# Kernel optimization log

Measured on AMD Instinct MI355X. Metric: run time of the kernel, lower is better.

Reference implementation:

```python
import jax, jax.numpy as jnp
import numpy as np

N_ATOMS = 8192
N_PAIRS = 65536
F = 128        # n_atombasis
R = 20         # n_radialbasis
B = 5          # graph_n_blocks
EPS = 1e-8     # stability constant


def setup_inputs() -> dict:
    key = jax.random.key(0)
    ks = jax.random.split(key, 16)
    rn = lambda k, shape, s=0.05: jax.random.normal(k, shape, dtype=jnp.float32) * s
    return {
        "features": jax.random.normal(ks[0], (N_ATOMS, F), jnp.float32),
        "distances": jax.random.uniform(ks[1], (N_PAIRS,), jnp.float32, 0.5, 5.0),
        "vectors": jax.random.normal(ks[2], (N_PAIRS, 3), jnp.float32),
        "cutoffs": jax.random.uniform(ks[3], (N_PAIRS,), jnp.float32),
        "rbfs": jax.random.normal(ks[4], (N_PAIRS, R), jnp.float32),
        "filter_W": rn(ks[5], (R, B * 3 * F)),
        "filter_b": jnp.zeros((B * 3 * F,), jnp.float32),
        "int_W1": rn(ks[6], (B, F, F)),
        "int_b1": jnp.zeros((B, F), jnp.float32),
        "int_W2": rn(ks[7], (B, F, 3 * F)),
        "int_b2": jnp.zeros((B, 3 * F), jnp.float32),
        "mix_Wv": rn(ks[8], (B, F, 2 * F)),
        "mix_W1": rn(ks[9], (B, 2 * F, F)),
        "mix_b1": jnp.zeros((B, F), jnp.float32),
        "mix_W2": rn(ks[10], (B, F, 3 * F)),
        "mix_b2": jnp.zeros((B, 3 * F), jnp.float32),
        "idx_i": jax.random.randint(ks[11], (N_PAIRS,), 0, N_ATOMS),
        "idx_j": jax.random.randint(ks[12], (N_PAIRS,), 0, N_ATOMS),
    }


def reference(features, distances, vectors, cutoffs, rbfs,
              filter_W, filter_b, int_W1, int_b1, int_W2, int_b2,
              mix_Wv, mix_W1, mix_b1, mix_W2, mix_b2, idx_i, idx_j):
    n_atoms = features.shape[0]
    # Cutoff-weighted radial filters, one (3F) chunk per block: [P, B*3F]
    descriptors = (rbfs @ filter_W + filter_b) * cutoffs[:, None]
    dir_ij = vectors / distances[:, None]                       # [P, 3]

    q = features[:, None, :]                                    # [N, 1, F]
    mu = jnp.zeros((n_atoms, 3, F), dtype=features.dtype)       # [N, 3, F]

    for b in range(B):
        # --- interaction block ---
        x = jax.nn.silu(q @ int_W1[b] + int_b1[b]) @ int_W2[b] + int_b2[b]  # [N,1,3F]
        Wij = descriptors[:, None, b * 3 * F:(b + 1) * 3 * F]               # [P,1,3F]
        xj = x[idx_j] * Wij                                                 # [P,1,3F]
        muj = mu[idx_j]                                                     # [P,3,F]
        dq, dmuR, dmumu = jnp.split(xj, 3, axis=-1)                         # [P,1,F] each
        dmu = dmuR * dir_ij[:, :, None] + dmumu * muj                       # [P,3,F]
        q = q + jax.ops.segment_sum(dq, idx_i, num_segments=n_atoms)
        mu = mu + jax.ops.segment_sum(dmu, idx_i, num_segments=n_atoms)

        # --- mixing block ---
        mu_V, mu_W = jnp.split(mu @ mix_Wv[b], 2, axis=-1)                  # [N,3,F] each
        mu_Vn = jnp.sqrt(jnp.sum(mu_V ** 2, axis=-2, keepdims=True) + EPS)  # [N,1,F]
        ctx = jnp.concatenate([q, mu_Vn], axis=-1)                          # [N,1,2F]
        y = jax.nn.silu(ctx @ mix_W1[b] + mix_b1[b]) @ mix_W2[b] + mix_b2[b]
        dq_i, dmu_i, dqmu_i = jnp.split(y, 3, axis=-1)                      # [N,1,F] each
        q = q + dq_i + dqmu_i * jnp.sum(mu_V * mu_W, axis=1, keepdims=True)
        mu = mu + dmu_i * mu_W

    return q[:, 0, :], mu
```

## Files before the change

### kernel.cpp

```cpp
#include <hip/hip_runtime.h>
#include <hip/hip_bf16.h>

#define NA 8192
#define NP 65536
#define WROW 1920

typedef short short8 __attribute__((ext_vector_type(8)));
typedef short short4v __attribute__((ext_vector_type(4)));
typedef float floatx4 __attribute__((ext_vector_type(4)));
typedef unsigned uint3v __attribute__((ext_vector_type(3)));

static __device__ __forceinline__ short f2bf(float f) {
    union { float f; unsigned u; } v; v.f = f;
    unsigned r = v.u + 0x7FFF + ((v.u >> 16) & 1);
    return (short)(r >> 16);
}
static __device__ __forceinline__ float bf2f(short s) {
    union { unsigned u; float f; } v;
    v.u = ((unsigned)(unsigned short)s) << 16;
    return v.f;
}
static __device__ __forceinline__ unsigned char f2fp8(float f) {
    int p = __builtin_amdgcn_cvt_pk_fp8_f32(f, 0.f, 0, false);
    return (unsigned char)(p & 0xFF);
}
static __device__ __forceinline__ float fp82f(unsigned char b) {
    return __builtin_amdgcn_cvt_f32_fp8((int)b, 0);
}
static __device__ __forceinline__ float silu(float v) {
    return v / (1.f + __expf(-v));
}

static __device__ __forceinline__ void swz(const float* __restrict__ src,
                                           short* __restrict__ dst,
                                           int K, int N, int idx) {
    int kn = K * N;
    int b = idx / kn;
    int r = idx - b * kn;
    int tile = r >> 9, li = r & 511;
    int lane = li >> 3, bb = li & 7;
    int Kt = K >> 5;
    int nt = tile / Kt, kt = tile - nt * Kt;
    int k = kt * 32 + (lane >> 4) * 8 + bb;
    int n = nt * 16 + (lane & 15);
    dst[idx] = f2bf(src[b * kn + k * N + n]);
}

__global__ __launch_bounds__(256) void k_tconv_all(const float* __restrict__ iW1,
                                                   const float* __restrict__ iW2,
                                                   const float* __restrict__ mWv,
                                                   const float* __restrict__ mW1,
                                                   const float* __restrict__ mW2,
                                                   const float* __restrict__ fW,
                                                   short* __restrict__ W1t,
                                                   short* __restrict__ W2t,
                                                   short* __restrict__ Wvt,
                                                   short* __restrict__ mW1t,
                                                   short* __restrict__ mW2t,
                                                   short* __restrict__ fWt) {
    int idx = blockIdx.x * 256 + threadIdx.x;
    if (idx < 81920)       { swz(iW1, W1t, 128, 128, idx); return; }
    idx -= 81920;
    if (idx < 245760)      { swz(iW2, W2t, 128, 384, idx); return; }
    idx -= 245760;
    if (idx < 163840)      { swz(mWv, Wvt, 128, 256, idx); return; }
    idx -= 163840;
    if (idx < 163840)      { swz(mW1, mW1t, 256, 128, idx); return; }
    idx -= 163840;
    if (idx < 245760)      { swz(mW2, mW2t, 128, 384, idx); return; }
    idx -= 245760;
    if (idx < 61440) {
        int b = idx / 12288;
        int r = idx - b * 12288;
        int nt = r >> 9;
        int li = r & 511;
        int lane = li >> 3, bb = li & 7;
        int k = (lane >> 4) * 8 + bb;
        int n = nt * 16 + (lane & 15);
        fWt[idx] = (k < 20) ? f2bf(fW[k * WROW + b * 384 + n]) : (short)0;
    }
}

__global__ __launch_bounds__(256) void k_init(const float* __restrict__ feat,
                                              float* __restrict__ q,
                                              float* __restrict__ mu,
                                              short* __restrict__ q_bf,
                                              unsigned* __restrict__ xmu_u,
                                              int* __restrict__ counts,
                                              int* __restrict__ cursor,
                                              float* __restrict__ cut_csr,
                                              short* __restrict__ rbf_c) {
    int idx = blockIdx.x * 256 + threadIdx.x;
    if (idx < NA * 128) { float v = feat[idx]; q[idx] = v; q_bf[idx] = f2bf(v); }
    mu[idx] = 0.f;
    xmu_u[idx] = 0;
    if (idx < NA) { counts[idx] = 0; cursor[idx] = 0; }
    if (idx < 16) {
        cut_csr[NP + idx] = 0.f;
        #pragma unroll
        for (int k = 0; k < 32; ++k) rbf_c[(NP + idx) * 32 + k] = 0;
    }
}

__global__ __launch_bounds__(256) void k_hist(const int* __restrict__ idx_i,
                                              int* __restrict__ counts) {
    int p = blockIdx.x * 256 + threadIdx.x;
    if (p < NP) atomicAdd(&counts[idx_i[p]], 1);
}

__global__ __launch_bounds__(1024) void k_scan(const int* __restrict__ counts,
                                               int* __restrict__ offs) {
    __shared__ int sums[1024];
    int t = threadIdx.x;
    int local[8];
    int s = 0;
    #pragma unroll
    for (int k = 0; k < 8; ++k) { local[k] = s; s += counts[t * 8 + k]; }
    sums[t] = s;
    __syncthreads();
    for (int off = 1; off < 1024; off <<= 1) {
        int v = sums[t];
        int u = (t >= off) ? sums[t - off] : 0;
        __syncthreads();
        sums[t] = v + u;
        __syncthreads();
    }
    int base = (t > 0) ? sums[t - 1] : 0;
    #pragma unroll
    for (int k = 0; k < 8; ++k) offs[t * 8 + k] = base + local[k];
    if (t == 1023) offs[NA] = sums[1023];
}

__global__ __launch_bounds__(256) void k_fillprep(const int* __restrict__ idx_i,
                                                  const int* __restrict__ idx_j,
                                                  const int* __restrict__ offs,
                                                  int* __restrict__ cursor,
                                                  const float* __restrict__ cut,
                                                  const float* __restrict__ dist,
                                                  const float* __restrict__ vec,
                                                  const float* __restrict__ rbfs,
                                                  int* __restrict__ jcsr,
                                                  float* __restrict__ cut_csr,
                                                  float4* __restrict__ dir_csr,
                                                  short* __restrict__ rbf_c) {
    int p = blockIdx.x * 256 + threadIdx.x;
    if (p >= NP) return;
    int i = idx_i[p];
    int pos = atomicAdd(&cursor[i], 1);
    int e = offs[i] + pos;
    jcsr[e] = idx_j[p];
    float c = cut[p];
    cut_csr[e] = c;
    float invd = 1.f / dist[p];
    float4 d;
    d.x = vec[p * 3 + 0] * invd;
    d.y = vec[p * 3 + 1] * invd;
    d.z = vec[p * 3 + 2] * invd;
    d.w = 0.f;
    dir_csr[e] = d;
    #pragma unroll
    for (int k = 0; k < 20; ++k) rbf_c[e * 32 + k] = f2bf(rbfs[p * 20 + k] * c);
    #pragma unroll
    for (int k = 20; k < 32; ++k) rbf_c[e * 32 + k] = 0;
}

__global__ __launch_bounds__(256) void k_x(const short* __restrict__ q_bf,
                                           const short* __restrict__ W1sw,
                                           const short* __restrict__ W2sw,
                                           const float* __restrict__ b1,
                                           const float* __restrict__ b2,
                                           unsigned char* __restrict__ xmu) {
    __shared__ __align__(16) short qtile[16 * 136];
    __shared__ __align__(16) short hs[16 * 136];
    int t = threadIdx.x;
    int wv = t >> 6, lane = t & 63, quad = lane >> 4, l16 = lane & 15;
    int a0 = blockIdx.x * 16;

    #pragma unroll
    for (int it = 0; it < 2; ++it) {
        int c = it * 256 + t;
        int row = c >> 5, col4 = c & 31;
        *(short4v*)(qtile + row * 136 + col4 * 4) =
            *(const short4v*)(q_bf + (a0 + row) * 128 + col4 * 4);
    }
    __syncthreads();

    floatx4 acc0 = {0.f, 0.f, 0.f, 0.f}, acc1 = {0.f, 0.f, 0.f, 0.f};
    #pragma unroll
    for (int kk = 0; kk < 4; ++kk) {
        short8 a  = *(const short8*)(qtile + l16 * 136 + kk * 32 + quad * 8);
        short8 b0 = *(const short8*)(W1sw + ((wv * 2 + 0) * 4 + kk) * 512 + lane * 8);
        short8 bq = *(const short8*)(W1sw + ((wv * 2 + 1) * 4 + kk) * 512 + lane * 8);
        acc0 = __builtin_amdgcn_mfma_f32_16x16x32_bf16(a, b0, acc0, 0, 0, 0);
        acc1 = __builtin_amdgcn_mfma_f32_16x16x32_bf16(a, bq, acc1, 0, 0, 0);
    }
    __syncthreads();
    {
        int n0 = wv * 32 + l16;
        float bia0 = b1[n0], bia1 = b1[n0 + 16];
        #pragma unroll
        for (int r = 0; r < 4; ++r) {
            int m = quad * 4 + r;
            hs[m * 136 + n0]      = f2bf(silu(acc0[r] + bia0));
            hs[m * 136 + n0 + 16] = f2bf(silu(acc1[r] + bia1));
        }
    }
    __syncthreads();
    floatx4 acc[6];
    #pragma unroll
    for (int jj = 0; jj < 6; ++jj) acc[jj] = {0.f, 0.f, 0.f, 0.f};
    #pragma unroll
    for (int kk = 0; kk < 4; ++kk) {
        short8 a = *(const short8*)(hs + l16 * 136 + kk * 32 + quad * 8);
        #pragma unroll
        for (int jj = 0; jj < 6; ++jj) {
            short8 b = *(const short8*)(W2sw + ((wv * 6 + jj) * 4 + kk) * 512 + lane * 8);
            acc[jj] = __builtin_amdgcn_mfma_f32_16x16x32_bf16(a, b, acc[jj], 0, 0, 0);
        }
    }
    #pragma unroll
    for (int jj = 0; jj < 6; ++jj) {
        int n = wv * 96 + jj * 16 + l16;
        float bia = b2[n];
        #pragma unroll
        for (int r = 0; r < 4; ++r) {
            int m = quad * 4 + r;
            xmu[(size_t)((a0 + m) * 128 + (n & 127)) * 12 + (n >> 7)] =
                f2fp8(acc[jj][r] + bia);
        }
    }
}

__global__ __launch_bounds__(256, 6) void k_gather(const unsigned char* __restrict__ xmu,
                                                   const short* __restrict__ rbf_c,
                                                   const short* __restrict__ fWt,
                                                   const float* __restrict__ fbp,
                                                   const int* __restrict__ jcsr,
                                                   const float* __restrict__ cut_csr,
                                                   const float4* __restrict__ dir_csr,
                                                   const int* __restrict__ offs,
                                                   short* __restrict__ dqg,
                                                   short* __restrict__ dmug) {
    __shared__ short dlds[16 * 392];
    __shared__ float pm[4 * 128];
    int i = blockIdx.x;
    int t = threadIdx.x;
    int h = t >> 7;
    int f = t & 127;
    int wv = t >> 6, lane = t & 63, quad = lane >> 4, l16 = lane & 15;
    int start = offs[i], end = offs[i + 1];
    float qa = 0.f, m0a = 0.f, m1a = 0.f, m2a = 0.f;

    for (int e0 = start; e0 < end; e0 += 16) {
        if (e0 > start) __syncthreads();
        short8 a = *(const short8*)(rbf_c + (e0 + l16) * 32 + quad * 8);
        float c0 = cut_csr[e0 + quad * 4 + 0];
        float c1 = cut_csr[e0 + quad * 4 + 1];
        float c2 = cut_csr[e0 + quad * 4 + 2];
        float c3 = cut_csr[e0 + quad * 4 + 3];
        #pragma unroll
        for (int nt = 0; nt < 6; ++nt) {
            int col = wv * 96 + nt * 16 + l16;
            short8 bfr = *(const short8*)(fWt + (wv * 6 + nt) * 512 + lane * 8);
            floatx4 z = {0.f, 0.f, 0.f, 0.f};
            floatx4 acc = __builtin_amdgcn_mfma_f32_16x16x32_bf16(a, bfr, z, 0, 0, 0);
            float fbv = fbp[col];
            dlds[(quad * 4 + 0) * 392 + col] = f2bf(acc[0] + fbv * c0);
            dlds[(quad * 4 + 1) * 392 + col] = f2bf(acc[1] + fbv * c1);
            dlds[(quad * 4 + 2) * 392 + col] = f2bf(acc[2] + fbv * c2);
            dlds[(quad * 4 + 3) * 392 + col] = f2bf(acc[3] + fbv * c3);
        }
        __syncthreads();
        int lim = (end < e0 + 16) ? end : (e0 + 16);
        int e = e0 + h;
        if (e < lim) {
            int jA = jcsr[e];
            float4 dirA = dir_csr[e];
            uint3v recA = *(const uint3v*)(xmu + (size_t)jA * 1536 + f * 12);
            for (; e < lim; e += 2) {
                uint3v rec = recA;
                float4 cdir = dirA;
                int en = e + 2;
                if (en < lim) {
                    int jn = jcsr[en];
                    dirA = dir_csr[en];
                    recA = *(const uint3v*)(xmu + (size_t)jn * 1536 + f * 12);
                }
                float x0 = fp82f((unsigned char)(rec.x & 0xFF));
                float x1 = fp82f((unsigned char)((rec.x >> 8) & 0xFF));
                float x2 = fp82f((unsigned char)((rec.x >> 16) & 0xFF));
                float u0 = bf2f((short)(rec.y & 0xFFFF));
                float u1 = bf2f((short)(rec.y >> 16));
                float u2 = bf2f((short)(rec.z & 0xFFFF));
                int le = e - e0;
                float wa = bf2f(dlds[le * 392 + f]);
                float wb = bf2f(dlds[le * 392 + 128 + f]);
                float wc = bf2f(dlds[le * 392 + 256 + f]);
                qa += x0 * wa;
                float xb = x1 * wb;
                float xc = x2 * wc;
                m0a += xb * cdir.x + xc * u0;
                m1a += xb * cdir.y + xc * u1;
                m2a += xb * cdir.z + xc * u2;
            }
        }
    }
    if (h == 1) {
        pm[0 * 128 + f] = qa;
        pm[1 * 128 + f] = m0a;
        pm[2 * 128 + f] = m1a;
        pm[3 * 128 + f] = m2a;
    }
    __syncthreads();
    if (h == 0) {
        qa  += pm[0 * 128 + f];
        m0a += pm[1 * 128 + f];
        m1a += pm[2 * 128 + f];
        m2a += pm[3 * 128 + f];
        dqg[i * 128 + f]             = f2bf(qa);
        dmug[(i * 3 + 0) * 128 + f]  = f2bf(m0a);
        dmug[(i * 3 + 1) * 128 + f]  = f2bf(m1a);
        dmug[(i * 3 + 2) * 128 + f]  = f2bf(m2a);
    }
}

__global__ __launch_bounds__(512, 6) void k_mixx(const float* __restrict__ mu_ro,
                                                 const short* __restrict__ dmug,
                                                 const float* __restrict__ q_ro,
                                                 const short* __restrict__ dqg,
                                                 const short* __restrict__ Wvsw,
                                                 const short* __restrict__ W1sw,
                                                 const short* __restrict__ W2sw,
                                                 const float* __restrict__ b1,
                                                 const float* __restrict__ b2,
                                                 float* __restrict__ q,
                                                 float* __restrict__ mu,
                                                 unsigned char* __restrict__ xmu,
                                                 const short* __restrict__ xW1sw,
                                                 const short* __restrict__ xW2sw,
                                                 const float* __restrict__ xb1,
                                                 const float* __restrict__ xb2,
                                                 int do_x) {
    __shared__ __align__(16) char smem[51968];
    short* ms    = (short*)(smem);
    short* qtile = (short*)(smem + 13056);
    short* Vv    = (short*)(smem + 17408);
    short* hs    = (short*)(smem + 17408);
    short* Vw    = (short*)(smem + 30464);
    short* vnb   = (short*)(smem + 43520);
    short* sb    = (short*)(smem + 47872);
    int t = threadIdx.x;
    int wv = t >> 6, lane = t & 63, quad = lane >> 4, l16 = lane & 15;
    int a0 = blockIdx.x * 16;

    #pragma unroll
    for (int k = 0; k < 12; ++k) {
        int idx = k * 512 + t;
        int row = idx >> 7, c = idx & 127;
        int g = (a0 * 3 + row) * 128 + c;
        ms[row * 136 + c] = f2bf(mu_ro[g] + bf2f(dmug[g]));
    }
    #pragma unroll
    for (int k = 0; k < 4; ++k) {
        int idx = k * 512 + t;
        int row = idx >> 7, c = idx & 127;
        int g = (a0 + row) * 128 + c;
        qtile[row * 136 + c] = f2bf(q_ro[g] + bf2f(dqg[g]));
    }
    __syncthreads();

    {
        floatx4 acc[3][2];
        #pragma unroll
        for (int mt = 0; mt < 3; ++mt)
            #pragma unroll
            for (int nt = 0; nt < 2; ++nt) acc[mt][nt] = {0.f, 0.f, 0.f, 0.f};
        #pragma unroll
        for (int kk = 0; kk < 4; ++kk) {
            short8 a[3];
            #pragma unroll
            for (int mt = 0; mt < 3; ++mt)
                a[mt] = *(const short8*)(ms + (mt * 16 + l16) * 136 + kk * 32 + quad * 8);
            #pragma unroll
            for (int nt = 0; nt < 2; ++nt) {
                short8 b = *(const short8*)(Wvsw + ((wv * 2 + nt) * 4 + kk) * 512 + lane * 8);
                #pragma unroll
                for (int mt = 0; mt < 3; ++mt)
                    acc[mt][nt] = __builtin_amdgcn_mfma_f32_16x16x32_bf16(a[mt], b, acc[mt][nt], 0, 0, 0);
            }
        }
        #pragma unroll
        for (int mt = 0; mt < 3; ++mt)
            #pragma unroll
            for (int nt = 0; nt < 2; ++nt)
                #pragma unroll
                for (int r = 0; r < 4; ++r) {
                    int row = mt * 16 + quad * 4 + r;
                    int col = wv * 32 + nt * 16 + l16;
                    short v = f2bf(acc[mt][nt][r]);
                    if (col < 128) Vv[row * 136 + col] = v;
                    else           Vw[row * 136 + col - 128] = v;
                }
    }
    __syncthreads();
    #pragma unroll
    for (int k = 0; k < 4; ++k) {
        int idx = k * 512 + t;
        int a = idx >> 7, c = idx & 127;
        float v0 = bf2f(Vv[(a * 3 + 0) * 136 + c]);
        float v1 = bf2f(Vv[(a * 3 + 1) * 136 + c]);
        float v2 = bf2f(Vv[(a * 3 + 2) * 136 + c]);
        float w0 = bf2f(Vw[(a * 3 + 0) * 136 + c]);
        float w1 = bf2f(Vw[(a * 3 + 1) * 136 + c]);
        float w2 = bf2f(Vw[(a * 3 + 2) * 136 + c]);
        vnb[a * 136 + c] = f2bf(sqrtf(v0 * v0 + v1 * v1 + v2 * v2 + 1e-8f));
        sb[a * 128 + c]  = f2bf(v0 * w0 + v1 * w1 + v2 * w2);
    }
    __syncthreads();
    {
        floatx4 acc0 = {0.f, 0.f, 0.f, 0.f};
        #pragma unroll
        for (int kk = 0; kk < 8; ++kk) {
            short8 a;
            if (kk < 4)
                a = *(const short8*)(qtile + l16 * 136 + kk * 32 + quad * 8);
            else
                a = *(const short8*)(vnb + l16 * 136 + (kk - 4) * 32 + quad * 8);
            short8 b0 = *(const short8*)(W1sw + (wv * 8 + kk) * 512 + lane * 8);
            acc0 = __builtin_amdgcn_mfma_f32_16x16x32_bf16(a, b0, acc0, 0, 0, 0);
        }
        int n0 = wv * 16 + l16;
        float bia0 = b1[n0];
        #pragma unroll
        for (int r = 0; r < 4; ++r) {
            int m = quad * 4 + r;
            hs[m * 136 + n0] = f2bf(silu(acc0[r] + bia0));
        }
    }
    __syncthreads();
    {
        floatx4 accB[3];
        #pragma unroll
        for (int c = 0; c < 3; ++c) accB[c] = {0.f, 0.f, 0.f, 0.f};
        #pragma unroll
        for (int kk = 0; kk < 4; ++kk) {
            short8 a = *(const short8*)(hs + l16 * 136 + kk * 32 + quad * 8);
            #pragma unroll
            for (int c = 0; c < 3; ++c) {
                short8 b = *(const short8*)(W2sw + ((c * 8 + wv) * 4 + kk) * 512 + lane * 8);
                accB[c] = __builtin_amdgcn_mfma_f32_16x16x32_bf16(a, b, accB[c], 0, 0, 0);
            }
        }
        int co = wv * 16 + l16;
        float bq_  = b2[co];
        float bm_  = b2[128 + co];
        float bqm_ = b2[256 + co];
        #pragma unroll
        for (int r = 0; r < 4; ++r) {
            int m = quad * 4 + r;
            int ga = a0 + m;
            float dq   = accB[0][r] + bq_;
            float dmu  = accB[1][r] + bm_;
            float dqmu = accB[2][r] + bqm_;
            float sv = bf2f(sb[m * 128 + co]);
            int gq = ga * 128 + co;
            float qn = (q[gq] + bf2f(dqg[gq])) + dq + dqmu * sv;
            q[gq] = qn;
            qtile[m * 136 + co] = f2bf(qn);
            #pragma unroll
            for (int d = 0; d < 3; ++d) {
                int gm = (ga * 3 + d) * 128 + co;
                float mw = bf2f(Vw[(m * 3 + d) * 136 + co]);
                float mn = (mu[gm] + bf2f(dmug[gm])) + dmu * mw;
                mu[gm] = mn;
                *(short*)(xmu + (size_t)gq * 12 + 4 + 2 * d) = f2bf(mn);
            }
        }
    }
    if (!do_x) return;
    __syncthreads();
    {
        floatx4 acc0 = {0.f, 0.f, 0.f, 0.f};
        #pragma unroll
        for (int kk = 0; kk < 4; ++kk) {
            short8 a  = *(const short8*)(qtile + l16 * 136 + kk * 32 + quad * 8);
            short8 b0 = *(const short8*)(xW1sw + (wv * 4 + kk) * 512 + lane * 8);
            acc0 = __builtin_amdgcn_mfma_f32_16x16x32_bf16(a, b0, acc0, 0, 0, 0);
        }
        int n0 = wv * 16 + l16;
        float bia0 = xb1[n0];
        #pragma unroll
        for (int r = 0; r < 4; ++r) {
            int m = quad * 4 + r;
            hs[m * 136 + n0] = f2bf(silu(acc0[r] + bia0));
        }
    }
    __syncthreads();
    {
        floatx4 acc[3];
        #pragma unroll
        for (int jj = 0; jj < 3; ++jj) acc[jj] = {0.f, 0.f, 0.f, 0.f};
        #pragma unroll
        for (int kk = 0; kk < 4; ++kk) {
            short8 a = *(const short8*)(hs + l16 * 136 + kk * 32 + quad * 8);
            #pragma unroll
            for (int jj = 0; jj < 3; ++jj) {
                short8 b = *(const short8*)(xW2sw + ((wv * 3 + jj) * 4 + kk) * 512 + lane * 8);
                acc[jj] = __builtin_amdgcn_mfma_f32_16x16x32_bf16(a, b, acc[jj], 0, 0, 0);
            }
        }
        #pragma unroll
        for (int jj = 0; jj < 3; ++jj) {
            int n = wv * 48 + jj * 16 + l16;
            float bia = xb2[n];
            #pragma unroll
            for (int r = 0; r < 4; ++r) {
                int m = quad * 4 + r;
                xmu[(size_t)((a0 + m) * 128 + (n & 127)) * 12 + (n >> 7)] =
                    f2fp8(acc[jj][r] + bia);
            }
        }
    }
}

extern "C" void kernel_launch(void* const* d_in, const int* in_sizes, int n_in,
                              void* d_out, int out_size, void* d_ws, size_t ws_size,
                              hipStream_t stream) {
    const float* feat = (const float*)d_in[0];
    const float* dist = (const float*)d_in[1];
    const float* vec  = (const float*)d_in[2];
    const float* cut  = (const float*)d_in[3];
    const float* rbfs = (const float*)d_in[4];
    const float* fW   = (const float*)d_in[5];
    const float* fb   = (const float*)d_in[6];
    const float* iW1  = (const float*)d_in[7];
    const float* ib1  = (const float*)d_in[8];
    const float* iW2  = (const float*)d_in[9];
    const float* ib2  = (const float*)d_in[10];
    const float* mWv  = (const float*)d_in[11];
    const float* mW1  = (const float*)d_in[12];
    const float* mb1  = (const float*)d_in[13];
    const float* mW2  = (const float*)d_in[14];
    const float* mb2  = (const float*)d_in[15];
    const int* idx_i  = (const int*)d_in[16];
    const int* idx_j  = (const int*)d_in[17];

    float* q  = (float*)d_out;
    float* mu = (float*)d_out + NA * 128;

    char* w = (char*)d_ws;
    unsigned char* xmu = (unsigned char*)(w);
    short* dqg     = (short*)(w + 12582912);
    short* q_bf    = (short*)(w + 14680064);
    short* dmug    = (short*)(w + 16777216);
    short* W1t     = (short*)(w + 23068672);
    short* W2t     = (short*)(w + 23232512);
    short* Wvt     = (short*)(w + 23724032);
    short* mW1t    = (short*)(w + 24051712);
    short* mW2t    = (short*)(w + 24379392);
    short* fWt     = (short*)(w + 24870912);
    int*   counts  = (int*)(w + 24993792);
    int*   cursor  = (int*)(w + 25026560);
    int*   offs    = (int*)(w + 25059328);
    int*   jcsr    = (int*)(w + 25092112);
    float* cut_csr = (float*)(w + 25354256);
    float4* dir_csr= (float4*)(w + 25616464);
    short* rbf_c   = (short*)(w + 26665040);

    k_tconv_all<<<(962560 + 255) / 256, 256, 0, stream>>>(iW1, iW2, mWv, mW1, mW2, fW,
                                                          W1t, W2t, Wvt, mW1t, mW2t, fWt);
    k_init<<<NA * 384 / 256, 256, 0, stream>>>(feat, q, mu, q_bf, (unsigned*)xmu,
                                               counts, cursor, cut_csr, rbf_c);
    k_hist<<<NP / 256, 256, 0, stream>>>(idx_i, counts);
    k_scan<<<1, 1024, 0, stream>>>(counts, offs);
    k_fillprep<<<NP / 256, 256, 0, stream>>>(idx_i, idx_j, offs, cursor, cut, dist, vec,
                                             rbfs, jcsr, cut_csr, dir_csr, rbf_c);

    k_x<<<NA / 16, 256, 0, stream>>>(q_bf, W1t, W2t, ib1, ib2, xmu);
    for (int b = 0; b < 5; ++b) {
        int bn = (b + 1) % 5;
        k_gather<<<NA, 256, 0, stream>>>(xmu, rbf_c, fWt + b * 12288,
                                         fb + b * 384, jcsr, cut_csr, dir_csr,
                                         offs, dqg, dmug);
        k_mixx<<<NA / 16, 512, 0, stream>>>(mu, dmug, q, dqg,
                                            Wvt + b * 32768,
                                            mW1t + b * 32768, mW2t + b * 49152,
                                            mb1 + b * 128, mb2 + b * 384,
                                            q, mu, xmu,
                                            W1t + bn * 16384, W2t + bn * 49152,
                                            ib1 + bn * 128, ib2 + bn * 384,
                                            (b < 4) ? 1 : 0);
    }
}
```

Baseline: 415.6 us.

## Process two atoms per gather block and pack mu bf16 stores

The gather kernel now handles two destination atoms per 256-thread block, with each 128-thread half accumulating one atom's edges over the shared edge range. This replaces the even/odd edge split and the LDS cross-half reduction, and lets the filter MFMA tiles cover edges from both atoms so fewer tiles are partially empty. The cost is load imbalance between the two halves when the atoms have different degrees. Separately, the mixing kernel writes the first two bf16 mu values as one 32-bit store instead of two 16-bit stores.

```diff
diff --git a/kernel.cpp b/kernel.cpp
--- a/kernel.cpp
+++ b/kernel.cpp
@@ -242,17 +242,18 @@
                                                    short* __restrict__ dqg,
                                                    short* __restrict__ dmug) {
     __shared__ short dlds[16 * 392];
-    __shared__ float pm[4 * 128];
-    int i = blockIdx.x;
+    int blk = blockIdx.x;
     int t = threadIdx.x;
     int h = t >> 7;
     int f = t & 127;
     int wv = t >> 6, lane = t & 63, quad = lane >> 4, l16 = lane & 15;
+    int i = blk * 2 + h;
+    int start2 = offs[blk * 2], end2 = offs[blk * 2 + 2];
     int start = offs[i], end = offs[i + 1];
     float qa = 0.f, m0a = 0.f, m1a = 0.f, m2a = 0.f;
 
-    for (int e0 = start; e0 < end; e0 += 16) {
-        if (e0 > start) __syncthreads();
+    for (int e0 = start2; e0 < end2; e0 += 16) {
+        if (e0 > start2) __syncthreads();
         short8 a = *(const short8*)(rbf_c + (e0 + l16) * 32 + quad * 8);
         float c0 = cut_csr[e0 + quad * 4 + 0];
         float c1 = cut_csr[e0 + quad * 4 + 1];
@@ -271,19 +272,18 @@
             dlds[(quad * 4 + 3) * 392 + col] = f2bf(acc[3] + fbv * c3);
         }
         __syncthreads();
-        int lim = (end < e0 + 16) ? end : (e0 + 16);
-        int e = e0 + h;
-        if (e < lim) {
-            int jA = jcsr[e];
-            float4 dirA = dir_csr[e];
+        int lo = (start > e0) ? start : e0;
+        int hi = (end < e0 + 16) ? end : (e0 + 16);
+        if (lo < hi) {
+            int jA = jcsr[lo];
+            float4 dirA = dir_csr[lo];
             uint3v recA = *(const uint3v*)(xmu + (size_t)jA * 1536 + f * 12);
-            for (; e < lim; e += 2) {
+            for (int e = lo; e < hi; ++e) {
                 uint3v rec = recA;
                 float4 cdir = dirA;
-                int en = e + 2;
-                if (en < lim) {
-                    int jn = jcsr[en];
-                    dirA = dir_csr[en];
+                if (e + 1 < hi) {
+                    int jn = jcsr[e + 1];
+                    dirA = dir_csr[e + 1];
                     recA = *(const uint3v*)(xmu + (size_t)jn * 1536 + f * 12);
                 }
                 float x0 = fp82f((unsigned char)(rec.x & 0xFF));
@@ -305,23 +305,10 @@
             }
         }
     }
-    if (h == 1) {
-        pm[0 * 128 + f] = qa;
-        pm[1 * 128 + f] = m0a;
-        pm[2 * 128 + f] = m1a;
-        pm[3 * 128 + f] = m2a;
-    }
-    __syncthreads();
-    if (h == 0) {
-        qa  += pm[0 * 128 + f];
-        m0a += pm[1 * 128 + f];
-        m1a += pm[2 * 128 + f];
-        m2a += pm[3 * 128 + f];
-        dqg[i * 128 + f]             = f2bf(qa);
-        dmug[(i * 3 + 0) * 128 + f]  = f2bf(m0a);
-        dmug[(i * 3 + 1) * 128 + f]  = f2bf(m1a);
-        dmug[(i * 3 + 2) * 128 + f]  = f2bf(m2a);
-    }
+    dqg[i * 128 + f]             = f2bf(qa);
+    dmug[(i * 3 + 0) * 128 + f]  = f2bf(m0a);
+    dmug[(i * 3 + 1) * 128 + f]  = f2bf(m1a);
+    dmug[(i * 3 + 2) * 128 + f]  = f2bf(m2a);
 }
 
 __global__ __launch_bounds__(512, 6) void k_mixx(const float* __restrict__ mu_ro,
@@ -467,14 +454,18 @@
             float qn = (q[gq] + bf2f(dqg[gq])) + dq + dqmu * sv;
             q[gq] = qn;
             qtile[m * 136 + co] = f2bf(qn);
+            float mn[3];
             #pragma unroll
             for (int d = 0; d < 3; ++d) {
                 int gm = (ga * 3 + d) * 128 + co;
                 float mw = bf2f(Vw[(m * 3 + d) * 136 + co]);
-                float mn = (mu[gm] + bf2f(dmug[gm])) + dmu * mw;
-                mu[gm] = mn;
-                *(short*)(xmu + (size_t)gq * 12 + 4 + 2 * d) = f2bf(mn);
+                mn[d] = (mu[gm] + bf2f(dmug[gm])) + dmu * mw;
+                mu[gm] = mn[d];
             }
+            unsigned lo = (unsigned)(unsigned short)f2bf(mn[0]) |
+                          ((unsigned)(unsigned short)f2bf(mn[1]) << 16);
+            *(unsigned*)(xmu + (size_t)gq * 12 + 4) = lo;
+            *(short*)(xmu + (size_t)gq * 12 + 8) = f2bf(mn[2]);
         }
     }
     if (!do_x) return;
@@ -579,9 +570,9 @@
     k_x<<<NA / 16, 256, 0, stream>>>(q_bf, W1t, W2t, ib1, ib2, xmu);
     for (int b = 0; b < 5; ++b) {
         int bn = (b + 1) % 5;
-        k_gather<<<NA, 256, 0, stream>>>(xmu, rbf_c, fWt + b * 12288,
-                                         fb + b * 384, jcsr, cut_csr, dir_csr,
-                                         offs, dqg, dmug);
+        k_gather<<<NA / 2, 256, 0, stream>>>(xmu, rbf_c, fWt + b * 12288,
+                                             fb + b * 384, jcsr, cut_csr, dir_csr,
+                                             offs, dqg, dmug);
         k_mixx<<<NA / 16, 512, 0, stream>>>(mu, dmug, q, dqg,
                                             Wvt + b * 32768,
                                             mW1t + b * 32768, mW2t + b * 49152,
```

After: 428.7 us. 1.03x slower.
